# Kernel optimization log

Measured on AMD Instinct MI355X. Metric: run time of the kernel, lower is better.

Reference implementation:

```python
import jax, jax.numpy as jnp
import numpy as np

B, LQ, LA, H = 32, 1024, 1024, 512
NEG = -1e7


def setup_inputs() -> dict:
    key = jax.random.key(0)
    kq, ka, ku = jax.random.split(key, 3)
    q = jax.random.normal(kq, (B, LQ, H), dtype=jnp.float32)
    a = jax.random.normal(ka, (B, LA, H), dtype=jnp.float32)
    U = 0.02 * jax.random.normal(ku, (H, H), dtype=jnp.float32)  # init.normal(std=0.02)
    q_mask = jnp.ones((B, LQ, 1), dtype=jnp.float32)
    a_mask = jnp.ones((B, LA, 1), dtype=jnp.float32)
    return {"q": q, "a": a, "U": U, "q_mask": q_mask, "a_mask": a_mask}


def reference(q, a, U, q_mask, a_mask):
    # mask[b,i,j] = q_mask[b,i] * a_mask[b,j]  (nonzero => valid)
    mask = jnp.matmul(q_mask, jnp.swapaxes(a_mask, 1, 2)) > 0  # [B,LQ,LA] bool
    # bilinear score X = q @ U @ a^T
    qU = jnp.einsum('bqh,hk->bqk', q, U)
    X = jnp.einsum('bqk,bak->bqa', qU, a)  # [B,LQ,LA]
    X = jnp.where(mask, X, NEG)
    I = jax.nn.sigmoid(X)
    att_a2q = jnp.max(jax.nn.softmax(I, axis=-1), axis=-1)  # [B,LQ]
    att_q2a = jnp.max(jax.nn.softmax(I, axis=-2), axis=-2)  # [B,LA]
    q_attn = jnp.einsum('blh,bl->bh', q, att_a2q)  # [B,H]
    a_attn = jnp.einsum('blh,bl->bh', a, att_q2a)  # [B,H]
    return q_attn, a_attn
```

## Files before the change

kernel.cpp:

```cpp
#include <hip/hip_runtime.h>

typedef __attribute__((ext_vector_type(8))) short bf16x8;
typedef __attribute__((ext_vector_type(4))) float f32x4;
typedef unsigned short u16;
typedef unsigned int u32;

#define NLOG2E -1.44269504088896f
#define LOG2E   1.44269504088896f
#define SLICE 32768

__device__ __forceinline__ float bf2f(u16 x) {
  union { u32 u; float f; } v; v.u = ((u32)x) << 16; return v.f;
}
__device__ __forceinline__ u16 f2b(float f) {
  union { float f; u32 u; } v; v.f = f;
  return (u16)((v.u + 0x7FFFu + ((v.u >> 16) & 1u)) >> 16);
}
__device__ __forceinline__ u32 pk2(float lo, float hi) {
  return (u32)f2b(lo) | ((u32)f2b(hi) << 16);
}
__device__ __forceinline__ bool inputs_are_bf16(const void* qmask) {
  return *(const u32*)qmask == 0x3F803F80u;
}

__device__ __forceinline__ void convert16(const void* __restrict__ src,
                                          u16* __restrict__ dst, int idx) {
  const float4* s = (const float4*)src + (size_t)idx * 4;
  float4 v0 = s[0], v1 = s[1], v2 = s[2], v3 = s[3];
  uint4* d = (uint4*)dst + (size_t)idx * 2;
  uint4 w0, w1;
  w0.x = pk2(v0.x, v0.y); w0.y = pk2(v0.z, v0.w);
  w0.z = pk2(v1.x, v1.y); w0.w = pk2(v1.z, v1.w);
  w1.x = pk2(v2.x, v2.y); w1.y = pk2(v2.z, v2.w);
  w1.z = pk2(v3.x, v3.y); w1.w = pk2(v3.z, v3.w);
  d[0] = w0;
  d[1] = w1;
}

__global__ __launch_bounds__(256) void prep_all(
    const void* __restrict__ q, const void* __restrict__ a,
    const void* __restrict__ U, const void* __restrict__ qmask,
    u16* __restrict__ qb, u16* __restrict__ ab, u16* __restrict__ Ut,
    float* __restrict__ out)
{
  const bool bf = inputs_are_bf16(qmask);
  const int t = threadIdx.x;
  const int bb = blockIdx.x;
  out[bb * 512 + t] = 0.f;
  out[bb * 512 + 256 + t] = 0.f;
  __shared__ u16 tile[64][65];
  const int bx = bb & 7, by = bb >> 3;
  #pragma unroll
  for (int i = 0; i < 16; i++) {
    int r = i * 4 + (t >> 6);
    int c = t & 63;
    size_t gi = (size_t)(by * 64 + r) * 512 + bx * 64 + c;
    tile[c][r] = bf ? ((const u16*)U)[gi] : f2b(((const float*)U)[gi]);
  }
  __syncthreads();
  #pragma unroll
  for (int i = 0; i < 16; i++) {
    int r = i * 4 + (t >> 6);
    int c = t & 63;
    Ut[(size_t)(bx * 64 + r) * 512 + by * 64 + c] = tile[r][c];
  }
}

template<int EPI, int AFP32>
__global__ __launch_bounds__(256, 3) void gemm_bt(
    const u16* __restrict__ A, const u16* __restrict__ B,
    u16* __restrict__ C, float scaleC,
    size_t strideA, size_t strideB,
    const void* __restrict__ q_mask, const void* __restrict__ a_mask,
    float* __restrict__ statsP,
    const u16* __restrict__ A_alias, const u16* __restrict__ B_alias,
    u16* __restrict__ wbA_dst,
    const void* __restrict__ convA_src, u16* __restrict__ convA_dst,
    const float* __restrict__ Af32)
{
  if constexpr (EPI == 0 && AFP32 == 1) {
    if (blockIdx.y >= 256) {
      const int cid = (blockIdx.y - 256) * 4 + blockIdx.x;
      convert16(convA_src, convA_dst, cid * 256 + (int)threadIdx.x);
      return;
    }
  }

  __shared__ __align__(16) char smem[50176];
  u16* Ct  = (u16*)smem;
  float* redS = (float*)smem;
  float* redM = (float*)(smem + 16896);
  float* colS = (float*)(smem + 33792);
  float* colM = (float*)(smem + 34816);
  float* qp = (float*)(smem + 49152);
  float* ap = (float*)(smem + 49664);

  int bx = blockIdx.x, by = blockIdx.y;
  const int bz = blockIdx.z;
  if (EPI) {
    const int k = blockIdx.x, s = blockIdx.y;
    bx = (k & 3) * 2 + (s & 1);
    by = (k >> 2) * 4 + (s >> 1);
  }
  const int tid  = threadIdx.x;
  const int lane = tid & 63;
  const int wave = tid >> 6;
  const int wr = wave >> 1, wc = wave & 1;
  const int l15 = lane & 15, lq = lane >> 4;

  const bool bfin = inputs_are_bf16(q_mask);
  const u16* Asel = (bfin && A_alias) ? A_alias : A;
  const u16* Bsel = (bfin && B_alias) ? B_alias : B;

  const int srl  = lane >> 2;
  const int sc   = (lane & 3) ^ ((lane >> 3) & 3);
  const size_t sgo = (size_t)srl * 512 + sc * 8;
  const int foff = ((lq ^ ((l15 >> 1) & 3)) * 8);

  const u16* Ab = Asel + strideA * bz + (size_t)by * 128 * 512;
  const u16* Bb = Bsel + strideB * bz + (size_t)bx * 128 * 512;

  if (EPI) {
    if (tid < 128) {
      int gi = bz * 1024 + by * 128 + tid;
      float v = bfin ? bf2f(((const u16*)q_mask)[gi]) : ((const float*)q_mask)[gi];
      qp[tid] = (v > 0.f) ? 0.f : 1e30f;
    } else {
      int gj = bz * 1024 + bx * 128 + (tid - 128);
      float v = bfin ? bf2f(((const u16*)a_mask)[gj]) : ((const float*)a_mask)[gj];
      ap[tid - 128] = (v > 0.f) ? 0.f : 1e30f;
    }
    __syncthreads();
  }

  f32x4 acc[4][4];
  if (EPI) {
    #pragma unroll
    for (int mt = 0; mt < 4; mt++)
      #pragma unroll
      for (int nt = 0; nt < 4; nt++) {
        float cp = ap[wc * 64 + nt * 16 + l15];
        #pragma unroll
        for (int r = 0; r < 4; r++)
          acc[mt][nt][r] = qp[wr * 64 + mt * 16 + lq * 4 + r] + cp;
      }
  } else {
    #pragma unroll
    for (int i = 0; i < 4; i++)
      #pragma unroll
      for (int j = 0; j < 4; j++) {
        f32x4 z = {0.f, 0.f, 0.f, 0.f};
        acc[i][j] = z;
      }
  }

  auto stageB = [&](int buf, int k0) {
    char* base = smem + buf * 16384 + 8192;
    #pragma unroll
    for (int i = 0; i < 2; i++) {
      const size_t go = (size_t)(wave * 32 + i * 16) * 512 + k0 + sgo;
      __builtin_amdgcn_global_load_lds(
          (const __attribute__((address_space(1))) void*)(Bb + go),
          (__attribute__((address_space(3))) void*)(base + wave * 2048 + i * 1024), 16, 0, 0);
    }
  };

  auto compute = [&](int t) {
    const u16* As = (const u16*)(smem + (t % 3) * 16384);
    const u16* Bs = As + 4096;
    bf16x8 af[4], bfr[4];
    #pragma unroll
    for (int tt = 0; tt < 4; tt++) {
      const int ar = wr * 64 + tt * 16 + l15;
      const int br = wc * 64 + tt * 16 + l15;
      af[tt]  = *(const bf16x8*)&As[ar * 32 + foff];
      bfr[tt] = *(const bf16x8*)&Bs[br * 32 + foff];
    }
    #pragma unroll
    for (int mt = 0; mt < 4; mt++)
      #pragma unroll
      for (int nt = 0; nt < 4; nt++)
        acc[mt][nt] = __builtin_amdgcn_mfma_f32_16x16x32_bf16(af[mt], bfr[nt], acc[mt][nt], 0, 0, 0);
  };

  if constexpr (AFP32) {
    const float* Ap = Af32 + (size_t)by * 128 * 512
                    + (size_t)(wave * 32 + srl) * 512 + sc * 8;
    float4 rs[3][4];
    auto issueStage = [&](int st) {
      const int k0 = st * 32;
      stageB(st % 3, k0);
      const float* p = Ap + k0;
      rs[st % 3][0] = *(const float4*)p;
      rs[st % 3][1] = *(const float4*)(p + 4);
      rs[st % 3][2] = *(const float4*)(p + 8192);
      rs[st % 3][3] = *(const float4*)(p + 8196);
    };
    auto writeA = [&](int t) {
      const int s = t % 3;
      uint4* dst = (uint4*)(smem + s * 16384 + wave * 2048 + lane * 16);
      uint4 w0, w1;
      w0.x = pk2(rs[s][0].x, rs[s][0].y); w0.y = pk2(rs[s][0].z, rs[s][0].w);
      w0.z = pk2(rs[s][1].x, rs[s][1].y); w0.w = pk2(rs[s][1].z, rs[s][1].w);
      w1.x = pk2(rs[s][2].x, rs[s][2].y); w1.y = pk2(rs[s][2].z, rs[s][2].w);
      w1.z = pk2(rs[s][3].x, rs[s][3].y); w1.w = pk2(rs[s][3].z, rs[s][3].w);
      dst[0]  = w0;
      dst[64] = w1;
      if (bx == 0) {
        u16* qrow = wbA_dst + (size_t)(by * 128 + wave * 32 + srl) * 512 + t * 32 + sc * 8;
        *(uint4*)qrow            = w0;
        *(uint4*)(qrow + 8192)   = w1;
      }
    };

    issueStage(0);
    issueStage(1);
    #pragma unroll
    for (int t = 0; t < 16; t++) {
      if (t + 2 < 16) issueStage(t + 2);
      if (t <= 13)      asm volatile("s_waitcnt vmcnt(12)" ::: "memory");
      else if (t == 14) asm volatile("s_waitcnt vmcnt(6)" ::: "memory");
      else              asm volatile("s_waitcnt vmcnt(0)" ::: "memory");
      writeA(t);
      asm volatile("s_waitcnt lgkmcnt(0)\n\ts_barrier" ::: "memory");
      compute(t);
      asm volatile("s_waitcnt lgkmcnt(0)\n\ts_barrier" ::: "memory");
    }
  } else {
    auto stage32 = [&](int buf, int k0) {
      char* base = smem + buf * 16384;
      #pragma unroll
      for (int i = 0; i < 2; i++) {
        const size_t go = (size_t)(wave * 32 + i * 16) * 512 + k0 + sgo;
        __builtin_amdgcn_global_load_lds(
            (const __attribute__((address_space(1))) void*)(Ab + go),
            (__attribute__((address_space(3))) void*)(base + wave * 2048 + i * 1024), 16, 0, 0);
        __builtin_amdgcn_global_load_lds(
            (const __attribute__((address_space(1))) void*)(Bb + go),
            (__attribute__((address_space(3))) void*)(base + 8192 + wave * 2048 + i * 1024), 16, 0, 0);
      }
    };
    stage32(0, 0);
    stage32(1, 32);
    #pragma unroll
    for (int t = 0; t < 16; t++) {
      if (t + 2 < 16) stage32((t + 2) % 3, (t + 2) * 32);
      if (t <= 13)      asm volatile("s_waitcnt vmcnt(8)\n\ts_barrier" ::: "memory");
      else if (t == 14) asm volatile("s_waitcnt vmcnt(4)\n\ts_barrier" ::: "memory");
      else              asm volatile("s_waitcnt vmcnt(0)\n\ts_barrier" ::: "memory");
      compute(t);
      asm volatile("s_waitcnt lgkmcnt(0)\n\ts_barrier" ::: "memory");
    }
  }

  if (!EPI) {
    #pragma unroll
    for (int mt = 0; mt < 4; mt++)
      #pragma unroll
      for (int nt = 0; nt < 4; nt++)
        #pragma unroll
        for (int r = 0; r < 4; r++) {
          int row = wr * 64 + mt * 16 + lq * 4 + r;
          int col = wc * 64 + nt * 16 + l15;
          Ct[row * 144 + col] = f2b(scaleC * acc[mt][nt][r]);
        }
    __syncthreads();
    u16* Cb = C + (size_t)by * 128 * 512 + bx * 128;
    #pragma unroll
    for (int i = 0; i < 8; i++) {
      int c = tid + i * 256;
      int row = c >> 4, cc = c & 15;
      *(bf16x8*)&Cb[(size_t)row * 512 + cc * 8] = *(const bf16x8*)&Ct[row * 144 + cc * 8];
    }
  } else {
    const int gi0 = bz * 1024 + by * 128;
    const int gj0 = bz * 1024 + bx * 128;
    float* rowsumP = statsP + 0      + bx * SLICE;
    float* colsumP = statsP + 262144 + by * SLICE;
    float* rowminP = statsP + 524288 + bx * SLICE;
    float* colminP = statsP + 786432 + by * SLICE;

    float csum[4] = {0.f, 0.f, 0.f, 0.f};
    float cmin[4] = {3e38f, 3e38f, 3e38f, 3e38f};
    #pragma unroll
    for (int mt = 0; mt < 4; mt++) {
      #pragma unroll
      for (int r = 0; r < 4; r++) {
        const int row = wr * 64 + mt * 16 + lq * 4 + r;
        float rsm = 0.f, rmn = 3e38f;
        #pragma unroll
        for (int nt = 0; nt < 4; nt++) {
          float y = acc[mt][nt][r];
          float u = __builtin_amdgcn_exp2f(y);
          float s = __builtin_amdgcn_rcpf(1.f + u);
          float e = __builtin_amdgcn_exp2f(LOG2E * s);
          rsm += e;
          csum[nt] += e;
          rmn = fminf(rmn, y);
          cmin[nt] = fminf(cmin[nt], y);
        }
        redS[row * 33 + l15 + 16 * wc] = rsm;
        redM[row * 33 + l15 + 16 * wc] = rmn;
      }
    }
    #pragma unroll
    for (int nt = 0; nt < 4; nt++) {
      float cs = csum[nt], cm = cmin[nt];
      cs += __shfl_xor(cs, 16); cm = fminf(cm, __shfl_xor(cm, 16));
      cs += __shfl_xor(cs, 32); cm = fminf(cm, __shfl_xor(cm, 32));
      if (lane < 16) {
        int j = wc * 64 + nt * 16 + l15;
        colS[j * 2 + wr] = cs;
        colM[j * 2 + wr] = cm;
      }
    }
    __syncthreads();
    if (tid < 128) {
      float s = 0.f;
      #pragma unroll
      for (int j = 0; j < 32; j++) s += redS[tid * 33 + j];
      rowsumP[gi0 + tid] = s;
      colsumP[gj0 + tid] = colS[tid * 2] + colS[tid * 2 + 1];
    } else {
      const int r = tid - 128;
      float m = 3e38f;
      #pragma unroll
      for (int j = 0; j < 32; j++) m = fminf(m, redM[r * 33 + j]);
      rowminP[gi0 + r] = m;
      colminP[gj0 + r] = fminf(colM[r * 2], colM[r * 2 + 1]);
    }
  }
}

__global__ __launch_bounds__(256) void partial_kernel(
    const u16* __restrict__ qb, const u16* __restrict__ ab,
    const void* __restrict__ q0, const void* __restrict__ a0,
    const void* __restrict__ qmask,
    const float* __restrict__ statsP, float* __restrict__ out)
{
  __shared__ float att[128];
  __shared__ float red[4][512];
  const int tid = threadIdx.x;
  const int seg = blockIdx.x;
  const int b = blockIdx.y >> 1, half = blockIdx.y & 1;
  if (tid < 128) {
    const int g = b * 1024 + seg * 128 + tid;
    const float* sumP = statsP + half * 262144;
    const float* minP = statsP + 524288 + half * 262144;
    float s = 0.f, m = 3e38f;
    #pragma unroll
    for (int s8 = 0; s8 < 8; s8++) {
      s += sumP[s8 * SLICE + g];
      m = fminf(m, minP[s8 * SLICE + g]);
    }
    float Imax = __builtin_amdgcn_rcpf(1.f + __builtin_amdgcn_exp2f(m));
    att[tid] = __expf(Imax) * __builtin_amdgcn_rcpf(s);
  }
  __syncthreads();
  const bool bf = inputs_are_bf16(qmask);
  const u16* base = bf ? (const u16*)(half ? a0 : q0) : (half ? ab : qb);
  const uint4* src = (const uint4*)(base + (size_t)b * 524288
                                    + (size_t)seg * 128 * 512);
  const int rw = tid >> 6;
  const int lane = tid & 63;
  float a0v = 0.f, a1v = 0.f, a2v = 0.f, a3v = 0.f;
  float a4v = 0.f, a5v = 0.f, a6v = 0.f, a7v = 0.f;
  #pragma unroll 8
  for (int i = 0; i < 32; i++) {
    const int row = i * 4 + rw;
    uint4 w = src[(size_t)row * 64 + lane];
    float wt = att[row];
    a0v = fmaf(__uint_as_float(w.x << 16), wt, a0v);
    a1v = fmaf(__uint_as_float(w.x & 0xFFFF0000u), wt, a1v);
    a2v = fmaf(__uint_as_float(w.y << 16), wt, a2v);
    a3v = fmaf(__uint_as_float(w.y & 0xFFFF0000u), wt, a3v);
    a4v = fmaf(__uint_as_float(w.z << 16), wt, a4v);
    a5v = fmaf(__uint_as_float(w.z & 0xFFFF0000u), wt, a5v);
    a6v = fmaf(__uint_as_float(w.w << 16), wt, a6v);
    a7v = fmaf(__uint_as_float(w.w & 0xFFFF0000u), wt, a7v);
  }
  *(float4*)&red[rw][lane * 8]     = make_float4(a0v, a1v, a2v, a3v);
  *(float4*)&red[rw][lane * 8 + 4] = make_float4(a4v, a5v, a6v, a7v);
  __syncthreads();
  const int h = tid * 2;
  float s0 = red[0][h]     + red[1][h]     + red[2][h]     + red[3][h];
  float s1 = red[0][h + 1] + red[1][h + 1] + red[2][h + 1] + red[3][h + 1];
  float* ob = out + half * 16384 + b * 512 + h;
  atomicAdd(&ob[0], s0);
  atomicAdd(&ob[1], s1);
}

extern "C" void kernel_launch(void* const* d_in, const int* in_sizes, int n_in,
                              void* d_out, int out_size, void* d_ws, size_t ws_size,
                              hipStream_t stream) {
  const void* q  = d_in[0];
  const void* a  = d_in[1];
  const void* U  = d_in[2];
  const void* qm = d_in[3];
  const void* am = d_in[4];
  float* out = (float*)d_out;

  char* ws = (char*)d_ws;
  u16* qb    = (u16*)ws;
  u16* ab    = (u16*)(ws + 33554432);
  u16* qU    = (u16*)(ws + 67108864);
  u16* Ut    = (u16*)(ws + 100663296);
  float* statsP = (float*)(ws + 100663296);

  const bool host_bf = (in_sizes[0] == 33554432);
  prep_all<<<dim3(64), dim3(256), 0, stream>>>(q, a, U, qm, qb, ab, Ut, out);
  if (host_bf) {
    gemm_bt<0, 0><<<dim3(4, 256, 1), dim3(256), 0, stream>>>(
        qb, Ut, qU, NLOG2E, (size_t)0, (size_t)0, qm, am, statsP,
        (const u16*)q, (const u16*)nullptr,
        nullptr, nullptr, nullptr, nullptr);
  } else {
    gemm_bt<0, 1><<<dim3(4, 1280, 1), dim3(256), 0, stream>>>(
        qb, Ut, qU, NLOG2E, (size_t)0, (size_t)0, qm, am, statsP,
        (const u16*)nullptr, (const u16*)nullptr,
        qb, a, ab, (const float*)q);
  }
  gemm_bt<1, 0><<<dim3(8, 8, 32), dim3(256), 0, stream>>>(
      qU, ab, (u16*)nullptr, 1.f, (size_t)524288, (size_t)524288, qm, am, statsP,
      (const u16*)nullptr, (const u16*)a,
      nullptr, nullptr, nullptr, nullptr);
  partial_kernel<<<dim3(8, 64), dim3(256), 0, stream>>>(qb, ab, q, a, qm, statsP, out);
}
```

Baseline: 257.1 us.

## Drop bf16 q copy, double-buffer GEMM pipeline, remap block tiles for locality

The first GEMM no longer writes a bf16 copy of q to workspace. The partial reduction now reads q directly in fp32, removing a write and a later read of the converted buffer. Both GEMM kernels go from triple to double buffering, which cuts shared memory so the launch bound rises to four blocks per CU, at the cost of less prefetch depth. Block indices are also remapped in both GEMMs to change tile scheduling order for cache locality, and the conversion blocks return early when inputs are already bf16.

New measurement: 253.3 us. No clear change (-1.5%).

```diff
diff --git a/kernel.cpp b/kernel.cpp
--- a/kernel.cpp
+++ b/kernel.cpp
@@ -38,10 +38,8 @@
 }
 
 __global__ __launch_bounds__(256) void prep_all(
-    const void* __restrict__ q, const void* __restrict__ a,
     const void* __restrict__ U, const void* __restrict__ qmask,
-    u16* __restrict__ qb, u16* __restrict__ ab, u16* __restrict__ Ut,
-    float* __restrict__ out)
+    u16* __restrict__ Ut, float* __restrict__ out)
 {
   const bool bf = inputs_are_bf16(qmask);
   const int t = threadIdx.x;
@@ -67,40 +65,50 @@
 }
 
 template<int EPI, int AFP32>
-__global__ __launch_bounds__(256, 3) void gemm_bt(
+__global__ __launch_bounds__(256, 4) void gemm_bt(
     const u16* __restrict__ A, const u16* __restrict__ B,
     u16* __restrict__ C, float scaleC,
     size_t strideA, size_t strideB,
     const void* __restrict__ q_mask, const void* __restrict__ a_mask,
     float* __restrict__ statsP,
     const u16* __restrict__ A_alias, const u16* __restrict__ B_alias,
-    u16* __restrict__ wbA_dst,
-    const void* __restrict__ convA_src, u16* __restrict__ convA_dst,
+    const void* __restrict__ conv_src, u16* __restrict__ conv_dst,
     const float* __restrict__ Af32)
 {
+  const bool bfin = inputs_are_bf16(q_mask);
+
   if constexpr (EPI == 0 && AFP32 == 1) {
     if (blockIdx.y >= 256) {
+      if (bfin) return;
       const int cid = (blockIdx.y - 256) * 4 + blockIdx.x;
-      convert16(convA_src, convA_dst, cid * 256 + (int)threadIdx.x);
+      convert16(conv_src, conv_dst, cid * 256 + (int)threadIdx.x);
       return;
     }
   }
 
-  __shared__ __align__(16) char smem[50176];
+  __shared__ __align__(16) char smem[37888];
   u16* Ct  = (u16*)smem;
   float* redS = (float*)smem;
   float* redM = (float*)(smem + 16896);
   float* colS = (float*)(smem + 33792);
   float* colM = (float*)(smem + 34816);
-  float* qp = (float*)(smem + 49152);
-  float* ap = (float*)(smem + 49664);
-
-  int bx = blockIdx.x, by = blockIdx.y;
-  const int bz = blockIdx.z;
+  float* qp = (float*)(smem + 36864);
+  float* ap = (float*)(smem + 37376);
+
+  int bx, by;
+  int bz = blockIdx.z;
   if (EPI) {
-    const int k = blockIdx.x, s = blockIdx.y;
-    bx = (k & 3) * 2 + (s & 1);
-    by = (k >> 2) * 4 + (s >> 1);
+    const int k = blockIdx.x;
+    const int s = blockIdx.y + 8 * (int)blockIdx.z;
+    bz = k * 4 + (s >> 6);
+    const int tt = s & 63;
+    bx = tt & 7;
+    by = tt >> 3;
+  } else {
+    const int F = (int)blockIdx.x + 4 * (int)blockIdx.y;
+    const int k = F & 7, jj = F >> 3;
+    bx = jj & 3;
+    by = k * 32 + (jj >> 2);
   }
   const int tid  = threadIdx.x;
   const int lane = tid & 63;
@@ -108,7 +116,6 @@
   const int wr = wave >> 1, wc = wave & 1;
   const int l15 = lane & 15, lq = lane >> 4;
 
-  const bool bfin = inputs_are_bf16(q_mask);
   const u16* Asel = (bfin && A_alias) ? A_alias : A;
   const u16* Bsel = (bfin && B_alias) ? B_alias : B;
 
@@ -166,7 +173,7 @@
   };
 
   auto compute = [&](int t) {
-    const u16* As = (const u16*)(smem + (t % 3) * 16384);
+    const u16* As = (const u16*)(smem + (t & 1) * 16384);
     const u16* Bs = As + 4096;
     bf16x8 af[4], bfr[4];
     #pragma unroll
@@ -183,50 +190,46 @@
         acc[mt][nt] = __builtin_amdgcn_mfma_f32_16x16x32_bf16(af[mt], bfr[nt], acc[mt][nt], 0, 0, 0);
   };
 
+  bool did_fp32 = false;
   if constexpr (AFP32) {
-    const float* Ap = Af32 + (size_t)by * 128 * 512
-                    + (size_t)(wave * 32 + srl) * 512 + sc * 8;
-    float4 rs[3][4];
-    auto issueStage = [&](int st) {
-      const int k0 = st * 32;
-      stageB(st % 3, k0);
-      const float* p = Ap + k0;
-      rs[st % 3][0] = *(const float4*)p;
-      rs[st % 3][1] = *(const float4*)(p + 4);
-      rs[st % 3][2] = *(const float4*)(p + 8192);
-      rs[st % 3][3] = *(const float4*)(p + 8196);
-    };
-    auto writeA = [&](int t) {
-      const int s = t % 3;
-      uint4* dst = (uint4*)(smem + s * 16384 + wave * 2048 + lane * 16);
-      uint4 w0, w1;
-      w0.x = pk2(rs[s][0].x, rs[s][0].y); w0.y = pk2(rs[s][0].z, rs[s][0].w);
-      w0.z = pk2(rs[s][1].x, rs[s][1].y); w0.w = pk2(rs[s][1].z, rs[s][1].w);
-      w1.x = pk2(rs[s][2].x, rs[s][2].y); w1.y = pk2(rs[s][2].z, rs[s][2].w);
-      w1.z = pk2(rs[s][3].x, rs[s][3].y); w1.w = pk2(rs[s][3].z, rs[s][3].w);
-      dst[0]  = w0;
-      dst[64] = w1;
-      if (bx == 0) {
-        u16* qrow = wbA_dst + (size_t)(by * 128 + wave * 32 + srl) * 512 + t * 32 + sc * 8;
-        *(uint4*)qrow            = w0;
-        *(uint4*)(qrow + 8192)   = w1;
-      }
-    };
-
-    issueStage(0);
-    issueStage(1);
-    #pragma unroll
-    for (int t = 0; t < 16; t++) {
-      if (t + 2 < 16) issueStage(t + 2);
-      if (t <= 13)      asm volatile("s_waitcnt vmcnt(12)" ::: "memory");
-      else if (t == 14) asm volatile("s_waitcnt vmcnt(6)" ::: "memory");
-      else              asm volatile("s_waitcnt vmcnt(0)" ::: "memory");
-      writeA(t);
-      asm volatile("s_waitcnt lgkmcnt(0)\n\ts_barrier" ::: "memory");
-      compute(t);
-      asm volatile("s_waitcnt lgkmcnt(0)\n\ts_barrier" ::: "memory");
-    }
-  } else {
+    if (!bfin) {
+      did_fp32 = true;
+      const float* Ap = Af32 + (size_t)by * 128 * 512
+                      + (size_t)(wave * 32 + srl) * 512 + sc * 8;
+      float4 rs[2][4];
+      auto issueStage = [&](int st) {
+        stageB(st & 1, st * 32);
+        const float* p = Ap + st * 32;
+        rs[st & 1][0] = *(const float4*)p;
+        rs[st & 1][1] = *(const float4*)(p + 4);
+        rs[st & 1][2] = *(const float4*)(p + 8192);
+        rs[st & 1][3] = *(const float4*)(p + 8196);
+      };
+      auto writeA = [&](int t) {
+        const int s = t & 1;
+        uint4* dst = (uint4*)(smem + s * 16384 + wave * 2048 + lane * 16);
+        uint4 w0, w1;
+        w0.x = pk2(rs[s][0].x, rs[s][0].y); w0.y = pk2(rs[s][0].z, rs[s][0].w);
+        w0.z = pk2(rs[s][1].x, rs[s][1].y); w0.w = pk2(rs[s][1].z, rs[s][1].w);
+        w1.x = pk2(rs[s][2].x, rs[s][2].y); w1.y = pk2(rs[s][2].z, rs[s][2].w);
+        w1.z = pk2(rs[s][3].x, rs[s][3].y); w1.w = pk2(rs[s][3].z, rs[s][3].w);
+        dst[0]  = w0;
+        dst[64] = w1;
+      };
+      issueStage(0);
+      #pragma unroll
+      for (int t = 0; t < 16; t++) {
+        if (t + 1 < 16) issueStage(t + 1);
+        if (t < 15) asm volatile("s_waitcnt vmcnt(6)" ::: "memory");
+        else        asm volatile("s_waitcnt vmcnt(0)" ::: "memory");
+        writeA(t);
+        asm volatile("s_waitcnt lgkmcnt(0)\n\ts_barrier" ::: "memory");
+        compute(t);
+        asm volatile("s_waitcnt lgkmcnt(0)\n\ts_barrier" ::: "memory");
+      }
+    }
+  }
+  if (!did_fp32) {
     auto stage32 = [&](int buf, int k0) {
       char* base = smem + buf * 16384;
       #pragma unroll
@@ -241,13 +244,11 @@
       }
     };
     stage32(0, 0);
-    stage32(1, 32);
     #pragma unroll
     for (int t = 0; t < 16; t++) {
-      if (t + 2 < 16) stage32((t + 2) % 3, (t + 2) * 32);
-      if (t <= 13)      asm volatile("s_waitcnt vmcnt(8)\n\ts_barrier" ::: "memory");
-      else if (t == 14) asm volatile("s_waitcnt vmcnt(4)\n\ts_barrier" ::: "memory");
-      else              asm volatile("s_waitcnt vmcnt(0)\n\ts_barrier" ::: "memory");
+      if (t + 1 < 16) stage32((t + 1) & 1, (t + 1) * 32);
+      if (t < 15) asm volatile("s_waitcnt vmcnt(4)\n\ts_barrier" ::: "memory");
+      else        asm volatile("s_waitcnt vmcnt(0)\n\ts_barrier" ::: "memory");
       compute(t);
       asm volatile("s_waitcnt lgkmcnt(0)\n\ts_barrier" ::: "memory");
     }
@@ -333,7 +334,7 @@
 }
 
 __global__ __launch_bounds__(256) void partial_kernel(
-    const u16* __restrict__ qb, const u16* __restrict__ ab,
+    const u16* __restrict__ ab,
     const void* __restrict__ q0, const void* __restrict__ a0,
     const void* __restrict__ qmask,
     const float* __restrict__ statsP, float* __restrict__ out)
@@ -358,26 +359,42 @@
   }
   __syncthreads();
   const bool bf = inputs_are_bf16(qmask);
-  const u16* base = bf ? (const u16*)(half ? a0 : q0) : (half ? ab : qb);
-  const uint4* src = (const uint4*)(base + (size_t)b * 524288
-                                    + (size_t)seg * 128 * 512);
   const int rw = tid >> 6;
   const int lane = tid & 63;
   float a0v = 0.f, a1v = 0.f, a2v = 0.f, a3v = 0.f;
   float a4v = 0.f, a5v = 0.f, a6v = 0.f, a7v = 0.f;
-  #pragma unroll 8
-  for (int i = 0; i < 32; i++) {
-    const int row = i * 4 + rw;
-    uint4 w = src[(size_t)row * 64 + lane];
-    float wt = att[row];
-    a0v = fmaf(__uint_as_float(w.x << 16), wt, a0v);
-    a1v = fmaf(__uint_as_float(w.x & 0xFFFF0000u), wt, a1v);
-    a2v = fmaf(__uint_as_float(w.y << 16), wt, a2v);
-    a3v = fmaf(__uint_as_float(w.y & 0xFFFF0000u), wt, a3v);
-    a4v = fmaf(__uint_as_float(w.z << 16), wt, a4v);
-    a5v = fmaf(__uint_as_float(w.z & 0xFFFF0000u), wt, a5v);
-    a6v = fmaf(__uint_as_float(w.w << 16), wt, a6v);
-    a7v = fmaf(__uint_as_float(w.w & 0xFFFF0000u), wt, a7v);
+  if (!bf && half == 0) {
+    const float4* src = (const float4*)q0 + (size_t)b * 131072
+                      + (size_t)seg * 16384;
+    #pragma unroll 8
+    for (int i = 0; i < 32; i++) {
+      const int row = i * 4 + rw;
+      float4 lo = src[(size_t)row * 128 + lane * 2];
+      float4 hi = src[(size_t)row * 128 + lane * 2 + 1];
+      float wt = att[row];
+      a0v = fmaf(lo.x, wt, a0v); a1v = fmaf(lo.y, wt, a1v);
+      a2v = fmaf(lo.z, wt, a2v); a3v = fmaf(lo.w, wt, a3v);
+      a4v = fmaf(hi.x, wt, a4v); a5v = fmaf(hi.y, wt, a5v);
+      a6v = fmaf(hi.z, wt, a6v); a7v = fmaf(hi.w, wt, a7v);
+    }
+  } else {
+    const u16* base = bf ? (const u16*)(half ? a0 : q0) : ab;
+    const uint4* src = (const uint4*)(base + (size_t)b * 524288
+                                      + (size_t)seg * 128 * 512);
+    #pragma unroll 8
+    for (int i = 0; i < 32; i++) {
+      const int row = i * 4 + rw;
+      uint4 w = src[(size_t)row * 64 + lane];
+      float wt = att[row];
+      a0v = fmaf(__uint_as_float(w.x << 16), wt, a0v);
+      a1v = fmaf(__uint_as_float(w.x & 0xFFFF0000u), wt, a1v);
+      a2v = fmaf(__uint_as_float(w.y << 16), wt, a2v);
+      a3v = fmaf(__uint_as_float(w.y & 0xFFFF0000u), wt, a3v);
+      a4v = fmaf(__uint_as_float(w.z << 16), wt, a4v);
+      a5v = fmaf(__uint_as_float(w.z & 0xFFFF0000u), wt, a5v);
+      a6v = fmaf(__uint_as_float(w.w << 16), wt, a6v);
+      a7v = fmaf(__uint_as_float(w.w & 0xFFFF0000u), wt, a7v);
+    }
   }
   *(float4*)&red[rw][lane * 8]     = make_float4(a0v, a1v, a2v, a3v);
   *(float4*)&red[rw][lane * 8 + 4] = make_float4(a4v, a5v, a6v, a7v);
@@ -401,28 +418,27 @@
   float* out = (float*)d_out;
 
   char* ws = (char*)d_ws;
-  u16* qb    = (u16*)ws;
   u16* ab    = (u16*)(ws + 33554432);
   u16* qU    = (u16*)(ws + 67108864);
   u16* Ut    = (u16*)(ws + 100663296);
   float* statsP = (float*)(ws + 100663296);
 
   const bool host_bf = (in_sizes[0] == 33554432);
-  prep_all<<<dim3(64), dim3(256), 0, stream>>>(q, a, U, qm, qb, ab, Ut, out);
+  prep_all<<<dim3(64), dim3(256), 0, stream>>>(U, qm, Ut, out);
   if (host_bf) {
     gemm_bt<0, 0><<<dim3(4, 256, 1), dim3(256), 0, stream>>>(
-        qb, Ut, qU, NLOG2E, (size_t)0, (size_t)0, qm, am, statsP,
+        (const u16*)q, Ut, qU, NLOG2E, (size_t)0, (size_t)0, qm, am, statsP,
         (const u16*)q, (const u16*)nullptr,
-        nullptr, nullptr, nullptr, nullptr);
+        nullptr, nullptr, nullptr);
   } else {
     gemm_bt<0, 1><<<dim3(4, 1280, 1), dim3(256), 0, stream>>>(
-        qb, Ut, qU, NLOG2E, (size_t)0, (size_t)0, qm, am, statsP,
-        (const u16*)nullptr, (const u16*)nullptr,
-        qb, a, ab, (const float*)q);
+        (const u16*)q, Ut, qU, NLOG2E, (size_t)0, (size_t)0, qm, am, statsP,
+        (const u16*)q, (const u16*)nullptr,
+        a, ab, (const float*)q);
   }
   gemm_bt<1, 0><<<dim3(8, 8, 32), dim3(256), 0, stream>>>(
       qU, ab, (u16*)nullptr, 1.f, (size_t)524288, (size_t)524288, qm, am, statsP,
       (const u16*)nullptr, (const u16*)a,
-      nullptr, nullptr, nullptr, nullptr);
-  partial_kernel<<<dim3(8, 64), dim3(256), 0, stream>>>(qb, ab, q, a, qm, statsP, out);
-}
+      nullptr, nullptr, nullptr);
+  partial_kernel<<<dim3(8, 64), dim3(256), 0, stream>>>(ab, q, a, qm, statsP, out);
+}
```
